# Performance work log

Measured on AMD Instinct MI355X. Metric: run time of the kernel, lower is better.

The kernel has to match this reference:

```python
import math
import jax, jax.numpy as jnp
import numpy as np

N_HEAD = 16
N_CLUSTER = 64
GROUP_SIZE = 256


def _sinusoidal(n, d):
    # emb[p, 2j] = sin(p*div_j), emb[p, 2j+1] = cos(p*div_j)  (interleaved, as in torch source)
    pos = jnp.arange(n, dtype=jnp.float32)[:, None]
    div = jnp.exp(jnp.arange(0, d, 2, dtype=jnp.float32) * (-math.log(10000.0) / d))
    ang = pos * div  # [n, d//2]
    return jnp.stack([jnp.sin(ang), jnp.cos(ang)], axis=-1).reshape(n, d)


def _rotary(pe, x):
    # Faithful to source: sin = first half of interleaved table, cos = second half,
    # and the function RETURNS ONLY the rotated term (not x*cos + rot*sin).
    d = x.shape[-1]
    sin, cos = pe[..., : d // 2], pe[..., d // 2 :]
    x_even, x_odd = x[..., ::2], x[..., 1::2]
    out = jnp.stack([-x_odd * cos, x_even * sin], axis=-1)
    return out.reshape(jnp.broadcast_shapes(x.shape[:-1] + (d // 2,), out.shape[:-1]) + (2,)).reshape(x.shape) if False else jnp.broadcast_to(out, x.shape[:-1] + (d // 2, 2)).reshape(x.shape)


def _forward(x, w_attn, b_attn, w_proj, b_proj, w_assign):
    B, T, C = x.shape
    H, nc, gs = N_HEAD, N_CLUSTER, GROUP_SIZE
    hd = C // H
    ntpc = T // nc                 # tokens per cluster
    G = T // gs                    # number of groups
    ncpg = gs // ntpc              # clusters summarized per group
    c_max = (G - 1) * ncpg         # max cluster-KV length (padded)

    qkv = x @ w_attn.T + b_attn    # [B, T, 3C]
    q, k, v = jnp.split(qkv, 3, axis=-1)

    # ---- soft cluster summarization (block-diagonal softmax over each cluster's tokens) ----
    x_r = x.reshape(B, nc, ntpc, C)
    logits = jnp.einsum('bctd,cd->bct', x_r, w_assign)        # only diagonal cluster survives the mask
    w = jax.nn.softmax(logits, axis=-1)                        # [B, nc, ntpc]
    ck = jnp.einsum('bct,bctd->bcd', w, k.reshape(B, nc, ntpc, C))  # [B, nc, C]
    cv = jnp.einsum('bct,bctd->bcd', w, v.reshape(B, nc, ntpc, C))

    # ---- split into groups & heads ----
    qg = q.reshape(B, G, gs, H, hd).transpose(0, 1, 3, 2, 4)   # [B,G,H,gs,hd]
    kl = k.reshape(B, G, gs, H, hd).transpose(0, 1, 3, 2, 4)
    vl = v.reshape(B, G, gs, H, hd).transpose(0, 1, 3, 2, 4)
    kc = ck[:, :c_max].reshape(B, c_max, H, hd)                # [B,c_max,H,hd]
    vc = cv[:, :c_max].reshape(B, c_max, H, hd)

    # ---- rotary (positions restart per group; cluster tokens occupy positions 0..c-1) ----
    S = _sinusoidal(c_max + gs, hd)
    qr = _rotary(S[:gs], qg)                                   # q positions 0..gs-1 in every group
    kcr = _rotary(S[:c_max, None, :], kc)                      # cluster slot j -> position j
    pos_local = jnp.arange(G)[:, None] * ncpg + jnp.arange(gs)[None, :]  # [G,gs]
    klr = _rotary(S[pos_local][None, :, None], kl)             # local key p in group g -> pos g*ncpg+p

    # ---- attention: cluster KV (fully visible, masked to first g*ncpg) + local causal ----
    scale = 1.0 / math.sqrt(hd)
    sc = jnp.einsum('bghqd,bchd->bghqc', qr, kcr) * scale      # [B,G,H,gs,c_max]
    sl = jnp.einsum('bghqd,bghkd->bghqk', qr, klr) * scale     # [B,G,H,gs,gs]
    cmask = jnp.arange(c_max)[None, :] < (jnp.arange(G) * ncpg)[:, None]  # [G,c_max]
    sc = jnp.where(cmask[None, :, None, None, :], sc, -jnp.inf)
    lmask = jnp.tril(jnp.ones((gs, gs), dtype=bool))
    sl = jnp.where(lmask, sl, -jnp.inf)
    p = jax.nn.softmax(jnp.concatenate([sc, sl], axis=-1), axis=-1)
    pc, pl = p[..., :c_max], p[..., c_max:]
    y = jnp.einsum('bghqc,bchd->bghqd', pc, vc) + jnp.einsum('bghqk,bghkd->bghqd', pl, vl)
    y = y.transpose(0, 1, 3, 2, 4).reshape(B, T, C)
    return y @ w_proj.T + b_proj


def setup_inputs() -> dict:
    key = jax.random.key(0)
    ks = jax.random.split(key, 4)
    B, T, C, NC = 4, 4096, 1024, N_CLUSTER
    x = jax.random.normal(ks[0], (B, T, C), jnp.float32)
    w_attn = jax.random.normal(ks[1], (3 * C, C), jnp.float32) * 0.02
    b_attn = jnp.zeros((3 * C,), jnp.float32)
    w_proj = jax.random.normal(ks[2], (C, C), jnp.float32) * 0.02
    b_proj = jnp.zeros((C,), jnp.float32)
    w_assign = jax.random.normal(ks[3], (NC, C), jnp.float32) * 0.02
    return {"x": x, "w_attn": w_attn, "b_attn": b_attn, "w_proj": w_proj, "b_proj": b_proj, "w_assign": w_assign}


def reference(x, w_attn, b_attn, w_proj, b_proj, w_assign):
    return _forward(x, w_attn, b_attn, w_proj, b_proj, w_assign)
```

## Files before the change

### kernel.cpp

```cpp
#include <hip/hip_runtime.h>
#include <stdint.h>

typedef unsigned short u16;
typedef unsigned int   u32;
typedef __attribute__((ext_vector_type(8))) short short8;
typedef __attribute__((ext_vector_type(4))) short short4v;
typedef __attribute__((ext_vector_type(4))) float float4v;
typedef __attribute__((ext_vector_type(4))) u32   uint4v;

#define B_  4
#define T_  4096
#define C_  1024
#define H_  16
#define G_  16
#define GS_ 256
#define NC_ 64

static __device__ __forceinline__ u16 f2bf(float f){
  union{float f; u32 u;} c; c.f = f;
  return (u16)((c.u + 0x7fffu + ((c.u >> 16) & 1u)) >> 16);
}
static __device__ __forceinline__ float bf2f(u16 u){
  union{u32 u; float f;} c; c.u = ((u32)u) << 16; return c.f;
}
static __device__ __forceinline__ void gload16(const void* g, void* l){
  __builtin_amdgcn_global_load_lds((__attribute__((address_space(1))) void*)g,
                                   (__attribute__((address_space(3))) void*)l, 16, 0, 0);
}
static __device__ __forceinline__ short8 rot8(short8 v, const float* Sp, int i0){
  union{ short8 s; u32 u[4]; } a, o; a.s = v;
  #pragma unroll
  for(int p = 0; p < 4; p++){
    float e0 = bf2f((u16)(a.u[p] & 0xffffu));
    float e1 = bf2f((u16)(a.u[p] >> 16));
    float sn = Sp[i0 + p], cs = Sp[32 + i0 + p];
    o.u[p] = (u32)f2bf(-e1 * cs) | ((u32)f2bf(e0 * sn) << 16);
  }
  return o.s;
}

__global__ __launch_bounds__(256) void init_kernel(const float* __restrict__ x,
    const float* __restrict__ wa, const float* __restrict__ wp,
    u16* __restrict__ xb, u16* __restrict__ wab, u16* __restrict__ wpb,
    float* __restrict__ S)
{
  const int bid = blockIdx.x;
  if(bid < 20480){
    int i = bid * 256 + threadIdx.x;
    const float* s; u16* d; int off;
    if(i < 4194304){ s = x; d = xb; off = i; }
    else if(i < 4980736){ s = wa; d = wab; off = i - 4194304; }
    else { s = wp; d = wpb; off = i - 4980736; }
    float4v v = *(const float4v*)(s + (size_t)off * 4);
    short4v o;
    o.x = (short)f2bf(v.x); o.y = (short)f2bf(v.y);
    o.z = (short)f2bf(v.z); o.w = (short)f2bf(v.w);
    *(short4v*)(d + (size_t)off * 4) = o;
  } else {
    int pos = (bid - 20480) * 4 + (threadIdx.x >> 6);
    int d = threadIdx.x & 63;
    if(pos < 316){
      int j = d >> 1;
      float div = __expf((float)(2 * j) * (-0.14391156831212787f));
      float ang = (float)pos * div;
      S[pos * 64 + d] = (d & 1) ? cosf(ang) : sinf(ang);
    }
  }
}

template<int MODE>
__global__ __launch_bounds__(512, 1) void gemm8p(const u16* __restrict__ A,
    const u16* __restrict__ Bm, const float* __restrict__ bias,
    void* __restrict__ Cv, u16* __restrict__ vtout, int M, int N, int K, int nbn)
{
  __shared__ u16 sA[2][2][256][32];
  __shared__ u16 sB[2][2][256][32];
  const int tid = threadIdx.x;
  const int lane = tid & 63, w = tid >> 6;
  const int l15 = lane & 15, l4 = lane >> 4;
  const int wr = w >> 2, wc = w & 3;

  const int cpx = gridDim.x >> 3;
  const int bid = blockIdx.x;
  const int swz = (bid & 7) * cpx + (bid >> 3);
  const int bm = swz / nbn, bn = swz - bm * nbn;
  const int row0 = bm * 256, col0 = bn * 256;

  float4v acc[8][4];
  #pragma unroll
  for(int m = 0; m < 8; m++)
    #pragma unroll
    for(int n = 0; n < 4; n++) acc[m][n] = (float4v){0.f, 0.f, 0.f, 0.f};

  const int srow = lane >> 2;
  const int sslot = lane & 3;

  auto stageHalfA = [&](u16* dstPlane, int ktOff){
    #pragma unroll
    for(int l = 0; l < 2; l++){
      int r = w * 32 + l * 16 + srow;
      int ss = sslot ^ ((r >> 1) & 3);
      const u16* src;
      if(MODE == 2){
        int bg = (row0 + r) >> 8;
        int hh = ktOff >> 6;
        int coff = (ktOff & 63) + ss * 8;
        src = A + ((size_t)(bg * 16 + hh)) * 16384 + (size_t)(r & 255) * 64 + coff;
      } else {
        src = A + (size_t)(row0 + r) * K + ktOff + ss * 8;
      }
      gload16(src, dstPlane + (w * 32 + l * 16) * 32);
    }
  };
  auto stageHalfB = [&](u16* dstPlane, int ktOff){
    #pragma unroll
    for(int l = 0; l < 2; l++){
      int r = w * 32 + l * 16 + srow;
      int ss = sslot ^ ((r >> 1) & 3);
      gload16(Bm + (size_t)(col0 + r) * K + ktOff + ss * 8,
              dstPlane + (w * 32 + l * 16) * 32);
    }
  };
  auto ldsReadA = [&](int d, int kk, int mh, short8* af){
    #pragma unroll
    for(int i = 0; i < 4; i++){
      int r = wr * 128 + (mh * 4 + i) * 16 + l15;
      int slot = l4 ^ ((r >> 1) & 3);
      af[i] = *(const short8*)&sA[d][kk][r][slot * 8];
    }
  };
  auto ldsReadB = [&](int d, int kk, short8* bf){
    #pragma unroll
    for(int i = 0; i < 4; i++){
      int r = wc * 64 + i * 16 + l15;
      int slot = l4 ^ ((r >> 1) & 3);
      bf[i] = *(const short8*)&sB[d][kk][r][slot * 8];
    }
  };
  auto mfma16 = [&](int mh, short8* af, short8* bf){
    __builtin_amdgcn_s_setprio(1);
    #pragma unroll
    for(int i = 0; i < 4; i++)
      #pragma unroll
      for(int n = 0; n < 4; n++)
        acc[mh * 4 + i][n] = __builtin_amdgcn_mfma_f32_16x16x32_bf16(af[i], bf[n], acc[mh * 4 + i][n], 0, 0, 0);
    __builtin_amdgcn_s_setprio(0);
  };

  stageHalfA(&sA[0][0][0][0], 0);
  stageHalfB(&sB[0][0][0][0], 0);
  stageHalfA(&sA[0][1][0][0], 32);
  stageHalfB(&sB[0][1][0][0], 32);
  asm volatile("s_waitcnt vmcnt(4)" ::: "memory");
  __builtin_amdgcn_s_barrier();

  const int nT = K >> 6;
  for(int t = 0; t < nT; t++){
    const int d = t & 1, dn = d ^ 1;
    const int ktN = (t + 1) << 6;
    const bool pf = (t + 1 < nT);
    short8 af[4], bf[4];

    ldsReadA(d, 0, 0, af); ldsReadB(d, 0, bf);
    if(pf) stageHalfA(&sA[dn][0][0][0], ktN);
    __builtin_amdgcn_s_barrier();
    mfma16(0, af, bf);
    __builtin_amdgcn_s_barrier();

    ldsReadA(d, 0, 1, af);
    if(pf) stageHalfB(&sB[dn][0][0][0], ktN);
    __builtin_amdgcn_s_barrier();
    mfma16(1, af, bf);
    if(pf) asm volatile("s_waitcnt vmcnt(4)" ::: "memory");
    else   asm volatile("s_waitcnt vmcnt(0)" ::: "memory");
    __builtin_amdgcn_s_barrier();

    ldsReadA(d, 1, 0, af); ldsReadB(d, 1, bf);
    if(pf) stageHalfA(&sA[dn][1][0][0], ktN + 32);
    __builtin_amdgcn_s_barrier();
    mfma16(0, af, bf);
    __builtin_amdgcn_s_barrier();

    ldsReadA(d, 1, 1, af);
    if(pf) stageHalfB(&sB[dn][1][0][0], ktN + 32);
    __builtin_amdgcn_s_barrier();
    mfma16(1, af, bf);
    if(pf) asm volatile("s_waitcnt vmcnt(4)" ::: "memory");
    __builtin_amdgcn_s_barrier();
  }

  #pragma unroll
  for(int m = 0; m < 8; m++){
    #pragma unroll
    for(int n = 0; n < 4; n++){
      int col = col0 + wc * 64 + n * 16 + l15;
      float bv = bias[col];
      #pragma unroll
      for(int j = 0; j < 4; j++){
        int row = row0 + wr * 128 + m * 16 + l4 * 4 + j;
        float v = acc[m][n][j] + bv;
        acc[m][n][j] = v;
        if(MODE == 1) ((u16*)Cv)[(size_t)row * N + col] = f2bf(v);
        else          ((float*)Cv)[(size_t)row * N + col] = v;
      }
    }
  }
  if(MODE == 1 && col0 >= 2048){
    const int b = row0 >> 12, g = (row0 >> 8) & 15;
    const int h = ((col0 - 2048) >> 6) + wc;
    u32* vbase = (u32*)(vtout + (((size_t)(b * 16 + g)) * 16 + h) * 16384);
    #pragma unroll
    for(int n = 0; n < 4; n++){
      int d = n * 16 + l15;
      #pragma unroll
      for(int m = 0; m < 8; m++){
        int kb = (wr * 128 + m * 16 + l4 * 4) >> 2;
        int col2 = (kb ^ (d & 7)) << 1;
        u32 lo = (u32)f2bf(acc[m][n][0]) | ((u32)f2bf(acc[m][n][1]) << 16);
        u32 hi = (u32)f2bf(acc[m][n][2]) | ((u32)f2bf(acc[m][n][3]) << 16);
        vbase[d * 128 + col2]     = lo;
        vbase[d * 128 + col2 + 1] = hi;
      }
    }
  }
}

__global__ __launch_bounds__(256) void cluster_kernel(
    const u16* __restrict__ xb, const float* __restrict__ wasn,
    const u16* __restrict__ qkv, const float* __restrict__ S,
    u16* __restrict__ ckr, u16* __restrict__ vct)
{
  const int bc = blockIdx.x;
  const int c = bc & 63, b = bc >> 6;
  const int tid = threadIdx.x;
  const int lane = tid & 63, wv = tid >> 6;
  __shared__ float wgt[64];

  const u16* xrow = xb + ((size_t)b * T_ + c * 64) * C_;
  float4v wa4[4];
  #pragma unroll
  for(int ch = 0; ch < 4; ch++)
    wa4[ch] = *(const float4v*)(wasn + c * C_ + ch * 256 + lane * 4);

  for(int it = 0; it < 16; it++){
    int t = it * 4 + wv;
    const u16* xr = xrow + (size_t)t * C_;
    float p = 0.f;
    #pragma unroll
    for(int ch = 0; ch < 4; ch++){
      short4v xv = *(const short4v*)(xr + ch * 256 + lane * 4);
      p += bf2f((u16)xv.x) * wa4[ch].x + bf2f((u16)xv.y) * wa4[ch].y
         + bf2f((u16)xv.z) * wa4[ch].z + bf2f((u16)xv.w) * wa4[ch].w;
    }
    p += __shfl_down(p, 32); p += __shfl_down(p, 16); p += __shfl_down(p, 8);
    p += __shfl_down(p, 4);  p += __shfl_down(p, 2);  p += __shfl_down(p, 1);
    if(lane == 0) wgt[t] = p;
  }
  __syncthreads();
  if(wv == 0){
    float v = wgt[lane];
    float mx = v;
    mx = fmaxf(mx, __shfl_xor(mx, 32)); mx = fmaxf(mx, __shfl_xor(mx, 16));
    mx = fmaxf(mx, __shfl_xor(mx, 8));  mx = fmaxf(mx, __shfl_xor(mx, 4));
    mx = fmaxf(mx, __shfl_xor(mx, 2));  mx = fmaxf(mx, __shfl_xor(mx, 1));
    float e = __expf(v - mx);
    float sm = e;
    sm += __shfl_xor(sm, 32); sm += __shfl_xor(sm, 16); sm += __shfl_xor(sm, 8);
    sm += __shfl_xor(sm, 4);  sm += __shfl_xor(sm, 2);  sm += __shfl_xor(sm, 1);
    wgt[lane] = e / sm;
  }
  __syncthreads();

  const int d0 = tid * 4;
  float ak[4] = {0, 0, 0, 0}, av[4] = {0, 0, 0, 0};
  const u16* krow = qkv + ((size_t)b * T_ + c * 64) * 3072 + C_ + d0;
  for(int t = 0; t < 64; t++){
    float wt = wgt[t];
    short4v kv = *(const short4v*)(krow + (size_t)t * 3072);
    short4v vv = *(const short4v*)(krow + (size_t)t * 3072 + C_);
    ak[0] += wt * bf2f((u16)kv.x); ak[1] += wt * bf2f((u16)kv.y);
    ak[2] += wt * bf2f((u16)kv.z); ak[3] += wt * bf2f((u16)kv.w);
    av[0] += wt * bf2f((u16)vv.x); av[1] += wt * bf2f((u16)vv.y);
    av[2] += wt * bf2f((u16)vv.z); av[3] += wt * bf2f((u16)vv.w);
  }
  const int dh = d0 & 63, i0 = dh >> 1;
  const float* Sp = S + c * 64;
  float s0 = Sp[i0],     c0 = Sp[32 + i0];
  float s1 = Sp[i0 + 1], c1 = Sp[32 + i0 + 1];
  short4v ck4;
  ck4.x = (short)f2bf(-ak[1] * c0); ck4.y = (short)f2bf(ak[0] * s0);
  ck4.z = (short)f2bf(-ak[3] * c1); ck4.w = (short)f2bf(ak[2] * s1);
  *(short4v*)(ckr + ((size_t)b * NC_ + c) * C_ + d0) = ck4;
  const int h = d0 >> 6;
  u16* vctb = vct + ((size_t)b * H_ + h) * 4096;
  #pragma unroll
  for(int i = 0; i < 4; i++){
    int d = dh + i;
    int col = ((c >> 2) ^ (d & 7)) * 4 + (c & 3);
    vctb[d * 64 + col] = f2bf(av[i]);
  }
}

__global__ __launch_bounds__(512, 2) void attn6_kernel(
    const u16* __restrict__ qkv, const u16* __restrict__ ckr,
    const u16* __restrict__ vct, u16* __restrict__ vt,
    const float* __restrict__ S)
{
  const int bid = blockIdx.x;
  const int h = bid & 15, g = (bid >> 4) & 15, b = bid >> 8;
  const int tid = threadIdx.x;
  const int lane = tid & 63, wv = tid >> 6;
  const int l15 = lane & 15, l4 = lane >> 4;
  const int rows0 = wv, rows1 = 15 - wv;

  __shared__ u16 SH[36864];
  u16* Ksh = SH;
  u16* Vsh = SH + 16384;
  u16* Vcl = SH + 32768;

  const size_t tok0 = (size_t)b * T_ + (size_t)g * GS_;
  u16* vslot = vt + (((size_t)b * 16 + g) * 16 + h) * 16384;

  {
    #pragma unroll
    for(int c = 0; c < 4; c++)
      gload16(vslot + (c * 512 + tid) * 8, Vsh + c * 4096 + wv * 512);
    gload16(vct + ((size_t)b * H_ + h) * 4096 + tid * 8, Vcl + wv * 512);
  }
  {
    const u16* kg = qkv + tok0 * 3072 + C_ + h * 64;
    #pragma unroll
    for(int c = 0; c < 4; c++){
      int idx = c * 512 + tid;
      int row = idx >> 3;
      int s0  = idx & 7;
      short8 v = *(const short8*)(kg + (size_t)row * 3072 + s0 * 8);
      short8 rv = rot8(v, S + (g * 4 + row) * 64, s0 * 4);
      *(short8*)(Ksh + row * 64 + (s0 ^ (row & 7)) * 8) = rv;
    }
  }
  short8 qa[2][2];
  #pragma unroll
  for(int f = 0; f < 2; f++){
    int rf = f ? rows1 : rows0;
    int qr = rf * 16 + l15;
    const u16* qp = qkv + (tok0 + qr) * 3072 + h * 64;
    #pragma unroll
    for(int kk = 0; kk < 2; kk++)
      qa[f][kk] = rot8(*(const short8*)(qp + kk * 32 + l4 * 8),
                       S + qr * 64, kk * 16 + l4 * 4);
  }
  __syncthreads();

  #pragma unroll
  for(int f = 0; f < 2; f++){
    const int rf = f ? rows1 : rows0;
    float4v o[4], osum;
    float mst = -1e30f;
    osum = (float4v){0, 0, 0, 0};
    #pragma unroll
    for(int n = 0; n < 4; n++) o[n] = (float4v){0, 0, 0, 0};

    auto sm_update = [&](float4v* st){
      float mx = st[0][0];
      #pragma unroll
      for(int n = 0; n < 4; n++)
        #pragma unroll
        for(int r = 0; r < 4; r++) mx = fmaxf(mx, st[n][r]);
      mx = fmaxf(mx, __shfl_xor(mx, 16));
      mx = fmaxf(mx, __shfl_xor(mx, 32));
      float mOld = mst;
      if(!__all(mx <= mOld)){
        float mn = fmaxf(mOld, mx);
        float rsc = __expf(mOld - mn);
        mst = mn;
        float r0 = __shfl(rsc, l4 * 4 + 0);
        float r1 = __shfl(rsc, l4 * 4 + 1);
        float r2 = __shfl(rsc, l4 * 4 + 2);
        float r3 = __shfl(rsc, l4 * 4 + 3);
        #pragma unroll
        for(int n = 0; n < 4; n++){
          o[n][0] *= r0; o[n][1] *= r1; o[n][2] *= r2; o[n][3] *= r3;
        }
        osum[0] *= r0; osum[1] *= r1; osum[2] *= r2; osum[3] *= r3;
      }
      float mm = mst;
      #pragma unroll
      for(int n = 0; n < 4; n++)
        #pragma unroll
        for(int r = 0; r < 4; r++) st[n][r] = __expf(st[n][r] - mm);
    };

    auto pv = [&](float4v* st, const u16* vb, int vstride, int granBase, int kbpMax){
      #pragma unroll
      for(int kbp = 0; kbp < 2; kbp++){
        if(kbp >= kbpMax) continue;
        union{ short8 s; u32 u[4]; } pa;
        pa.u[0] = (u32)f2bf(st[2*kbp][0])   | ((u32)f2bf(st[2*kbp][1]) << 16);
        pa.u[1] = (u32)f2bf(st[2*kbp][2])   | ((u32)f2bf(st[2*kbp][3]) << 16);
        pa.u[2] = (u32)f2bf(st[2*kbp+1][0]) | ((u32)f2bf(st[2*kbp+1][1]) << 16);
        pa.u[3] = (u32)f2bf(st[2*kbp+1][2]) | ((u32)f2bf(st[2*kbp+1][3]) << 16);
        union{ short8 s; u32 u[4]; } on;
        on.u[0] = 0x3F803F80u; on.u[1] = 0x3F803F80u;
        on.u[2] = 0x3F803F80u; on.u[3] = 0x3F803F80u;
        __builtin_amdgcn_s_setprio(1);
        osum = __builtin_amdgcn_mfma_f32_16x16x32_bf16(pa.s, on.s, osum, 0, 0, 0);
        #pragma unroll
        for(int dn = 0; dn < 4; dn++){
          int d = dn * 16 + l15;
          int gA = (granBase + (2*kbp) * 4 + l4) ^ (l15 & 7);
          int gB = (granBase + (2*kbp+1) * 4 + l4) ^ (l15 & 7);
          short4v vA = *(const short4v*)(vb + d * vstride + gA * 4);
          short4v vB = *(const short4v*)(vb + d * vstride + gB * 4);
          union{ short8 s; u32 u[4]; } vf;
          vf.u[0] = (u32)(u16)vA.x | ((u32)(u16)vA.y << 16);
          vf.u[1] = (u32)(u16)vA.z | ((u32)(u16)vA.w << 16);
          vf.u[2] = (u32)(u16)vB.x | ((u32)(u16)vB.y << 16);
          vf.u[3] = (u32)(u16)vB.z | ((u32)(u16)vB.w << 16);
          o[dn] = __builtin_amdgcn_mfma_f32_16x16x32_bf16(pa.s, vf.s, o[dn], 0, 0, 0);
        }
        __builtin_amdgcn_s_setprio(0);
      }
    };

    if(g > 0){
      const int climit = g * 4;
      const int nMaxC = (climit - 1) >> 4;
      const int kbpMaxC = (nMaxC >> 1) + 1;
      float4v st[4];
      #pragma unroll
      for(int n = 0; n < 4; n++) st[n] = (float4v){0, 0, 0, 0};
      #pragma unroll
      for(int kk = 0; kk < 2; kk++){
        __builtin_amdgcn_s_setprio(1);
        #pragma unroll
        for(int n = 0; n < 4; n++){
          if(n > nMaxC) continue;
          short8 kf = *(const short8*)(ckr + ((size_t)b * NC_ + n * 16 + l15) * C_
                                       + h * 64 + kk * 32 + l4 * 8);
          st[n] = __builtin_amdgcn_mfma_f32_16x16x32_bf16(kf, qa[f][kk], st[n], 0, 0, 0);
        }
        __builtin_amdgcn_s_setprio(0);
      }
      #pragma unroll
      for(int n = 0; n < 4; n++)
        #pragma unroll
        for(int r = 0; r < 4; r++){
          int col = n * 16 + l4 * 4 + r;
          st[n][r] = (col >= climit) ? -1e30f : st[n][r] * 0.125f;
        }
      sm_update(st);
      pv(st, Vcl, 64, 0, kbpMaxC);
    }

    const int ktF = rf >> 2;
    for(int kt = 0; kt <= ktF; kt++){
      const bool diag = (kt == ktF);
      const int nMax = diag ? (rf & 3) : 3;
      const int kbpMax = diag ? (((rf & 3) >> 1) + 1) : 2;
      float4v st[4];
      #pragma unroll
      for(int n = 0; n < 4; n++) st[n] = (float4v){0, 0, 0, 0};
      #pragma unroll
      for(int kk = 0; kk < 2; kk++){
        __builtin_amdgcn_s_setprio(1);
        #pragma unroll
        for(int n = 0; n < 4; n++){
          if(n > nMax) continue;
          int krow = kt * 64 + n * 16 + l15;
          int slot = (kk * 4 + l4) ^ (krow & 7);
          short8 kf = *(const short8*)(Ksh + krow * 64 + slot * 8);
          st[n] = __builtin_amdgcn_mfma_f32_16x16x32_bf16(kf, qa[f][kk], st[n], 0, 0, 0);
        }
        __builtin_amdgcn_s_setprio(0);
      }
      #pragma unroll
      for(int n = 0; n < 4; n++)
        #pragma unroll
        for(int r = 0; r < 4; r++){
          int col = kt * 64 + n * 16 + l4 * 4 + r;
          int q   = rf * 16 + l15;
          st[n][r] = (col > q) ? -1e30f : st[n][r] * 0.125f;
        }
      sm_update(st);
      pv(st, Vsh, 256, kt * 16, kbpMax);
    }

    #pragma unroll
    for(int r = 0; r < 4; r++){
      float inv = 1.0f / osum[r];
      int kq = rf * 16 + l4 * 4 + r;
      #pragma unroll
      for(int n = 0; n < 4; n++)
        vslot[kq * 64 + n * 16 + l15] = f2bf(o[n][r] * inv);
    }
  }
}

extern "C" void kernel_launch(void* const* d_in, const int* in_sizes, int n_in,
                              void* d_out, int out_size, void* d_ws, size_t ws_size,
                              hipStream_t stream)
{
  const float* x      = (const float*)d_in[0];
  const float* w_attn = (const float*)d_in[1];
  const float* b_attn = (const float*)d_in[2];
  const float* w_proj = (const float*)d_in[3];
  const float* b_proj = (const float*)d_in[4];
  const float* wasn   = (const float*)d_in[5];
  float* out = (float*)d_out;
  char* ws = (char*)d_ws;

  u16* qkv  = (u16*)(ws);
  u16* xb   = (u16*)(ws + 100663296);
  u16* vt   = (u16*)(ws + 134217728);
  u16* wab  = (u16*)(ws + 167772160);
  u16* wpb  = (u16*)(ws + 174063616);
  u16* ckr  = (u16*)(ws + 176160768);
  u16* vct  = (u16*)(ws + 176685056);
  float* st = (float*)(ws + 177209344);
  if(ws_size < 177290240) return;

  init_kernel<<<20559, 256, 0, stream>>>(x, w_attn, w_proj, xb, wab, wpb, st);
  gemm8p<1><<<768, 512, 0, stream>>>(xb, wab, b_attn, (void*)qkv, vt, 16384, 3072, 1024, 12);
  cluster_kernel<<<256, 256, 0, stream>>>(xb, wasn, qkv, st, ckr, vct);
  attn6_kernel<<<1024, 512, 0, stream>>>(qkv, ckr, vct, vt, st);
  gemm8p<2><<<256, 512, 0, stream>>>(vt, wpb, b_proj, (void*)out, nullptr, 16384, 1024, 1024, 4);
}
```

Baseline: 258.5 us.

## Fuse Q rotary into QKV GEMM epilogue and skip V row-major writes

The QKV GEMM epilogue now applies the rotary transform to Q columns, using a lane shuffle to fetch the even/odd partner, so the attention kernel loads Q without rotating it. V columns are no longer written row-major into qkv; only the transposed per-head V layout is stored, now with bias added. The cluster kernel reads V from that transposed layout with the swizzle applied. This removes redundant global stores and per-block rotary work, at the cost of more sin/cos table loads in the GEMM epilogue.

Result: slower. 316.7 us (+22.5%).

```diff
diff --git a/kernel.cpp b/kernel.cpp
--- a/kernel.cpp
+++ b/kernel.cpp
@@ -71,7 +71,8 @@
 template<int MODE>
 __global__ __launch_bounds__(512, 1) void gemm8p(const u16* __restrict__ A,
     const u16* __restrict__ Bm, const float* __restrict__ bias,
-    void* __restrict__ Cv, u16* __restrict__ vtout, int M, int N, int K, int nbn)
+    void* __restrict__ Cv, u16* __restrict__ vtout, const float* __restrict__ S,
+    int M, int N, int K, int nbn)
 {
   __shared__ u16 sA[2][2][256][32];
   __shared__ u16 sB[2][2][256][32];
@@ -189,35 +190,68 @@
     __builtin_amdgcn_s_barrier();
   }
 
-  #pragma unroll
-  for(int m = 0; m < 8; m++){
-    #pragma unroll
-    for(int n = 0; n < 4; n++){
-      int col = col0 + wc * 64 + n * 16 + l15;
-      float bv = bias[col];
-      #pragma unroll
-      for(int j = 0; j < 4; j++){
-        int row = row0 + wr * 128 + m * 16 + l4 * 4 + j;
-        float v = acc[m][n][j] + bv;
-        acc[m][n][j] = v;
-        if(MODE == 1) ((u16*)Cv)[(size_t)row * N + col] = f2bf(v);
-        else          ((float*)Cv)[(size_t)row * N + col] = v;
-      }
-    }
-  }
-  if(MODE == 1 && col0 >= 2048){
+  if(MODE == 2){
+    #pragma unroll
+    for(int m = 0; m < 8; m++)
+      #pragma unroll
+      for(int n = 0; n < 4; n++){
+        int col = col0 + wc * 64 + n * 16 + l15;
+        float bv = bias[col];
+        #pragma unroll
+        for(int j = 0; j < 4; j++){
+          int row = row0 + wr * 128 + m * 16 + l4 * 4 + j;
+          ((float*)Cv)[(size_t)row * N + col] = acc[m][n][j] + bv;
+        }
+      }
+    return;
+  }
+  if(col0 < 1024){
+    #pragma unroll
+    for(int m = 0; m < 8; m++)
+      #pragma unroll
+      for(int n = 0; n < 4; n++){
+        int col = col0 + wc * 64 + n * 16 + l15;
+        float bv = bias[col];
+        int i = (col & 63) >> 1;
+        #pragma unroll
+        for(int j = 0; j < 4; j++){
+          int row = row0 + wr * 128 + m * 16 + l4 * 4 + j;
+          float v = acc[m][n][j] + bv;
+          float p = __shfl_xor(v, 1);
+          int pos = row & 255;
+          float sn = S[pos * 64 + i];
+          float cs = S[pos * 64 + 32 + i];
+          float rv = (col & 1) ? p * sn : -p * cs;
+          ((u16*)Cv)[(size_t)row * N + col] = f2bf(rv);
+        }
+      }
+  } else if(col0 < 2048){
+    #pragma unroll
+    for(int m = 0; m < 8; m++)
+      #pragma unroll
+      for(int n = 0; n < 4; n++){
+        int col = col0 + wc * 64 + n * 16 + l15;
+        float bv = bias[col];
+        #pragma unroll
+        for(int j = 0; j < 4; j++){
+          int row = row0 + wr * 128 + m * 16 + l4 * 4 + j;
+          ((u16*)Cv)[(size_t)row * N + col] = f2bf(acc[m][n][j] + bv);
+        }
+      }
+  } else {
     const int b = row0 >> 12, g = (row0 >> 8) & 15;
     const int h = ((col0 - 2048) >> 6) + wc;
     u32* vbase = (u32*)(vtout + (((size_t)(b * 16 + g)) * 16 + h) * 16384);
     #pragma unroll
     for(int n = 0; n < 4; n++){
       int d = n * 16 + l15;
+      float bv = bias[col0 + wc * 64 + n * 16 + l15];
       #pragma unroll
       for(int m = 0; m < 8; m++){
         int kb = (wr * 128 + m * 16 + l4 * 4) >> 2;
         int col2 = (kb ^ (d & 7)) << 1;
-        u32 lo = (u32)f2bf(acc[m][n][0]) | ((u32)f2bf(acc[m][n][1]) << 16);
-        u32 hi = (u32)f2bf(acc[m][n][2]) | ((u32)f2bf(acc[m][n][3]) << 16);
+        u32 lo = (u32)f2bf(acc[m][n][0] + bv) | ((u32)f2bf(acc[m][n][1] + bv) << 16);
+        u32 hi = (u32)f2bf(acc[m][n][2] + bv) | ((u32)f2bf(acc[m][n][3] + bv) << 16);
         vbase[d * 128 + col2]     = lo;
         vbase[d * 128 + col2 + 1] = hi;
       }
@@ -227,7 +261,8 @@
 
 __global__ __launch_bounds__(256) void cluster_kernel(
     const u16* __restrict__ xb, const float* __restrict__ wasn,
-    const u16* __restrict__ qkv, const float* __restrict__ S,
+    const u16* __restrict__ qkv, const u16* __restrict__ vt,
+    const float* __restrict__ S,
     u16* __restrict__ ckr, u16* __restrict__ vct)
 {
   const int bc = blockIdx.x;
@@ -272,18 +307,35 @@
   __syncthreads();
 
   const int d0 = tid * 4;
-  float ak[4] = {0, 0, 0, 0}, av[4] = {0, 0, 0, 0};
+  const int dh = d0 & 63, h = d0 >> 6;
+
+  float ak[4] = {0, 0, 0, 0};
   const u16* krow = qkv + ((size_t)b * T_ + c * 64) * 3072 + C_ + d0;
   for(int t = 0; t < 64; t++){
     float wt = wgt[t];
     short4v kv = *(const short4v*)(krow + (size_t)t * 3072);
-    short4v vv = *(const short4v*)(krow + (size_t)t * 3072 + C_);
     ak[0] += wt * bf2f((u16)kv.x); ak[1] += wt * bf2f((u16)kv.y);
     ak[2] += wt * bf2f((u16)kv.z); ak[3] += wt * bf2f((u16)kv.w);
-    av[0] += wt * bf2f((u16)vv.x); av[1] += wt * bf2f((u16)vv.y);
-    av[2] += wt * bf2f((u16)vv.z); av[3] += wt * bf2f((u16)vv.w);
-  }
-  const int dh = d0 & 63, i0 = dh >> 1;
+  }
+  float av[4];
+  {
+    const u16* vtb = vt + (((size_t)b * 16 + (c >> 2)) * 16 + h) * 16384;
+    #pragma unroll
+    for(int i = 0; i < 4; i++){
+      int d = dh + i;
+      const u16* vrow = vtb + d * 256;
+      float a = 0.f;
+      #pragma unroll
+      for(int qq = 0; qq < 16; qq++){
+        int g2 = ((c & 3) * 16 + qq) ^ (d & 7);
+        short4v v4 = *(const short4v*)(vrow + g2 * 4);
+        a += wgt[qq * 4 + 0] * bf2f((u16)v4.x) + wgt[qq * 4 + 1] * bf2f((u16)v4.y)
+           + wgt[qq * 4 + 2] * bf2f((u16)v4.z) + wgt[qq * 4 + 3] * bf2f((u16)v4.w);
+      }
+      av[i] = a;
+    }
+  }
+  const int i0 = dh >> 1;
   const float* Sp = S + c * 64;
   float s0 = Sp[i0],     c0 = Sp[32 + i0];
   float s1 = Sp[i0 + 1], c1 = Sp[32 + i0 + 1];
@@ -291,7 +343,6 @@
   ck4.x = (short)f2bf(-ak[1] * c0); ck4.y = (short)f2bf(ak[0] * s0);
   ck4.z = (short)f2bf(-ak[3] * c1); ck4.w = (short)f2bf(ak[2] * s1);
   *(short4v*)(ckr + ((size_t)b * NC_ + c) * C_ + d0) = ck4;
-  const int h = d0 >> 6;
   u16* vctb = vct + ((size_t)b * H_ + h) * 4096;
   #pragma unroll
   for(int i = 0; i < 4; i++){
@@ -301,7 +352,7 @@
   }
 }
 
-__global__ __launch_bounds__(512, 2) void attn6_kernel(
+__global__ __launch_bounds__(512, 2) void attn7_kernel(
     const u16* __restrict__ qkv, const u16* __restrict__ ckr,
     const u16* __restrict__ vct, u16* __restrict__ vt,
     const float* __restrict__ S)
@@ -347,8 +398,7 @@
     const u16* qp = qkv + (tok0 + qr) * 3072 + h * 64;
     #pragma unroll
     for(int kk = 0; kk < 2; kk++)
-      qa[f][kk] = rot8(*(const short8*)(qp + kk * 32 + l4 * 8),
-                       S + qr * 64, kk * 16 + l4 * 4);
+      qa[f][kk] = *(const short8*)(qp + kk * 32 + l4 * 8);
   }
   __syncthreads();
 
@@ -521,8 +571,8 @@
   if(ws_size < 177290240) return;
 
   init_kernel<<<20559, 256, 0, stream>>>(x, w_attn, w_proj, xb, wab, wpb, st);
-  gemm8p<1><<<768, 512, 0, stream>>>(xb, wab, b_attn, (void*)qkv, vt, 16384, 3072, 1024, 12);
-  cluster_kernel<<<256, 256, 0, stream>>>(xb, wasn, qkv, st, ckr, vct);
-  attn6_kernel<<<1024, 512, 0, stream>>>(qkv, ckr, vct, vt, st);
-  gemm8p<2><<<256, 512, 0, stream>>>(vt, wpb, b_proj, (void*)out, nullptr, 16384, 1024, 1024, 4);
-}
+  gemm8p<1><<<768, 512, 0, stream>>>(xb, wab, b_attn, (void*)qkv, vt, st, 16384, 3072, 1024, 12);
+  cluster_kernel<<<256, 256, 0, stream>>>(xb, wasn, qkv, vt, st, ckr, vct);
+  attn7_kernel<<<1024, 512, 0, stream>>>(qkv, ckr, vct, vt, st);
+  gemm8p<2><<<256, 512, 0, stream>>>(vt, wpb, b_proj, (void*)out, nullptr, st, 16384, 1024, 1024, 4);
+}
```
